# Kernel optimization log

Hardware: AMD Instinct MI355X
Metric: run time of the kernel (lower is better)

Reference implementation:

```python
import jax, jax.numpy as jnp
import numpy as np

K = 5          # kernel_size
PAD = (K - 1) // 2  # fixed_padding with dilation=1, stride=1 -> 'same'


def setup_inputs() -> dict:
    key = jax.random.key(0)
    kx, kw = jax.random.split(key)
    x = jax.random.normal(kx, (4, 8, 512, 512), dtype=jnp.float32)
    # nn.Parameter initialized to zeros in the original; use small random values
    # so the op is non-trivial (math is identical for any weight values).
    weight = jax.random.normal(kw, (8, 8, K, K), dtype=jnp.float32) * 0.05
    return {"x": x, "weight": weight}


def reference(x, weight):
    """Morphological dilation2d with hard max (soft_max=False).

    out[n,o,h,w] = max_{c,dy,dx} ( x_pad[n,c,h+dy,w+dx] + weight[o,c,dy,dx] )
    Faithful to: pad zeros -> unfold -> weight + x -> max over dim C*k*k.
    Computed as a fused sliding-window max-plus reduction (no (N,C,k,k,H,W)
    unfold tensor is materialized; loop is over the fixed k*k kernel taps).
    """
    N, C, H, W = x.shape
    O = weight.shape[0]
    xp = jnp.pad(x, ((0, 0), (0, 0), (PAD, PAD), (PAD, PAD)))  # zero pad, as in F.pad
    out = jnp.full((N, O, H, W), -jnp.inf, dtype=x.dtype)
    for dy in range(K):
        for dx in range(K):
            patch = xp[:, :, dy:dy + H, dx:dx + W]           # (N,C,H,W)
            w_tap = weight[:, :, dy, dx]                      # (O,C)
            # (N,1,C,H,W) + (1,O,C,1,1) -> max over C -> (N,O,H,W)
            term = patch[:, None] + w_tap[None, :, :, None, None]
            out = jnp.maximum(out, jnp.max(term, axis=2))
    return out
```

## Files before the change

### kernel.cpp

```cpp
#include <hip/hip_runtime.h>
#include <math.h>
#include <stdint.h>

#define KK 5
#define PADK 2
#define C_IN 8
#define O_OUT 8
#define HH 512
#define WW 512
#define TH 8
#define TW 128
#define LROWS 12
#define LCOLS 136
#define WSTR 16
#define NW (O_OUT * C_IN * KK * KK)
#define XPAIRS (C_IN * LROWS * (LCOLS / 2))

static __device__ __forceinline__ float max3f(float a, float b, float c) {
    float d;
    asm("v_max3_f32 %0, %1, %2, %3" : "=v"(d) : "v"(a), "v"(b), "v"(c));
    return d;
}

__global__ __launch_bounds__(512, 2)
void dil_kernel(const float* __restrict__ x,
                const float* __restrict__ wf,
                float* __restrict__ out) {
    __shared__ __align__(16) float xlds[C_IN][LROWS][LCOLS];
    __shared__ __align__(16) float wlds[C_IN * 4 * KK * WSTR];

    const int tid = threadIdx.x;
    const int w0 = blockIdx.x * TW;
    const int h0 = blockIdx.y * TH;
    const int n  = blockIdx.z;

    const float* xn = x + (size_t)n * (C_IN * HH * WW);
    for (int idx = tid; idx < XPAIRS; idx += 512) {
        int c   = idx / (LROWS * (LCOLS / 2));
        int rem = idx - c * (LROWS * (LCOLS / 2));
        int r   = rem / (LCOLS / 2);
        int jp  = rem - r * (LCOLS / 2);
        int gh = h0 - PADK + r;
        int gw = w0 - PADK + 2 * jp;
        float v0 = 0.f, v1 = 0.f;
        if ((unsigned)gh < (unsigned)HH) {
            const float* row = xn + ((size_t)c * HH + gh) * WW;
            if ((unsigned)gw < (unsigned)WW) v0 = row[gw];
            if ((unsigned)(gw + 1) < (unsigned)WW) v1 = row[gw + 1];
        }
        float2* dst = (float2*)&xlds[c][r][2 * jp];
        *dst = make_float2(v0, v1);
    }
    for (int t = tid; t < NW; t += 512) {
        int dx = t % KK;  int q = t / KK;
        int o2 = q & 1;   q >>= 1;
        int dy = q % KK;  q /= KK;
        int og = q & 3;   int c = q >> 2;
        int o = og * 2 + o2;
        wlds[((c * 4 + og) * KK + dy) * WSTR + o2 * KK + dx] =
            wf[((o * C_IN + c) * KK + dy) * KK + dx];
    }
    __syncthreads();

    const int l   = tid & 63;
    const int wid = tid >> 6;
    const int og  = wid & 3;
    const int rq  = wid >> 2;
    const int rbase = rq * 4;

    float acc[2][4][2];
    #pragma unroll
    for (int a = 0; a < 2; ++a)
        #pragma unroll
        for (int j = 0; j < 4; ++j) {
            acc[a][j][0] = -INFINITY;
            acc[a][j][1] = -INFINITY;
        }

    for (int c = 0; c < C_IN; ++c) {
        float U[8][6];
        #pragma unroll
        for (int r = 0; r < 8; ++r) {
            const float* lr = &xlds[c][rbase + r][2 * l];
            float2 a = *(const float2*)(lr);
            float2 b = *(const float2*)(lr + 2);
            float2 d = *(const float2*)(lr + 4);
            U[r][0] = a.x; U[r][1] = a.y;
            U[r][2] = b.x; U[r][3] = b.y;
            U[r][4] = d.x; U[r][5] = d.y;
        }
        const float* wb = &wlds[(c * 4 + og) * KK * WSTR];
        #pragma unroll
        for (int dy = 0; dy < KK; ++dy) {
            const float* wch = wb + dy * WSTR;
            float4 wa = *(const float4*)(wch);
            float4 wv = *(const float4*)(wch + 4);
            float2 wc2 = *(const float2*)(wch + 8);
            float w[10] = {wa.x, wa.y, wa.z, wa.w,
                           wv.x, wv.y, wv.z, wv.w, wc2.x, wc2.y};
            #pragma unroll
            for (int o2 = 0; o2 < 2; ++o2) {
                #pragma unroll
                for (int j = 0; j < 4; ++j) {
                    const float* u = U[j + dy];
                    const float* wo = &w[o2 * 5];
                    {
                        float t0 = u[0] + wo[0], t1 = u[1] + wo[1],
                              t2 = u[2] + wo[2], t3 = u[3] + wo[3],
                              t4 = u[4] + wo[4];
                        acc[o2][j][0] = max3f(acc[o2][j][0],
                                              max3f(t0, t1, t2),
                                              fmaxf(t3, t4));
                    }
                    {
                        float t0 = u[1] + wo[0], t1 = u[2] + wo[1],
                              t2 = u[3] + wo[2], t3 = u[4] + wo[3],
                              t4 = u[5] + wo[4];
                        acc[o2][j][1] = max3f(acc[o2][j][1],
                                              max3f(t0, t1, t2),
                                              fmaxf(t3, t4));
                    }
                }
            }
        }
    }

    float* onp = out + (size_t)n * (O_OUT * HH * WW);
    const int hB = h0 + rbase;
    const int wcol = w0 + 2 * l;
    #pragma unroll
    for (int o2 = 0; o2 < 2; ++o2) {
        const int o = og * 2 + o2;
        #pragma unroll
        for (int j = 0; j < 4; ++j) {
            float2 rr = make_float2(acc[o2][j][0], acc[o2][j][1]);
            *(float2*)(&onp[((size_t)o * HH + hB + j) * WW + wcol]) = rr;
        }
    }
}

extern "C" void kernel_launch(void* const* d_in, const int* in_sizes, int n_in,
                              void* d_out, int out_size, void* d_ws, size_t ws_size,
                              hipStream_t stream) {
    const float* x   = (const float*)d_in[0];
    const float* wgt = (const float*)d_in[1];
    float* out = (float*)d_out;

    dim3 grid(WW / TW, HH / TH, 4);
    dim3 block(512);
    dil_kernel<<<grid, block, 0, stream>>>(x, wgt, out);
}
```

Before: 69.13 us.

## Stage input channels in two halves to shrink LDS and raise occupancy

Loads the input tile into shared memory four channels at a time in two passes, which halves the LDS footprint, and tightens the weight stride from 16 to 12. The x rows are now read from LDS for each (dy, j) instead of being cached in a per-channel register array, and launch bounds ask for 8 blocks per CU. The aim is to raise occupancy and hide global-load latency through more resident waves. The cost is an extra barrier, a second load phase, more LDS reads (20 rows per channel instead of 8), and a tighter register budget that could cause spills.

```diff
diff --git a/kernel.cpp b/kernel.cpp
--- a/kernel.cpp
+++ b/kernel.cpp
@@ -10,11 +10,12 @@
 #define WW 512
 #define TH 8
 #define TW 128
+#define CH 4
 #define LROWS 12
 #define LCOLS 136
-#define WSTR 16
+#define WSTR 12
 #define NW (O_OUT * C_IN * KK * KK)
-#define XPAIRS (C_IN * LROWS * (LCOLS / 2))
+#define XHALF (CH * LROWS * (LCOLS / 2))
 
 static __device__ __forceinline__ float max3f(float a, float b, float c) {
     float d;
@@ -22,45 +23,18 @@
     return d;
 }
 
-__global__ __launch_bounds__(512, 2)
+__global__ __launch_bounds__(512, 8)
 void dil_kernel(const float* __restrict__ x,
                 const float* __restrict__ wf,
                 float* __restrict__ out) {
-    __shared__ __align__(16) float xlds[C_IN][LROWS][LCOLS];
+    __shared__ __align__(16) float xlds[CH][LROWS][LCOLS];
     __shared__ __align__(16) float wlds[C_IN * 4 * KK * WSTR];
 
     const int tid = threadIdx.x;
     const int w0 = blockIdx.x * TW;
     const int h0 = blockIdx.y * TH;
     const int n  = blockIdx.z;
-
     const float* xn = x + (size_t)n * (C_IN * HH * WW);
-    for (int idx = tid; idx < XPAIRS; idx += 512) {
-        int c   = idx / (LROWS * (LCOLS / 2));
-        int rem = idx - c * (LROWS * (LCOLS / 2));
-        int r   = rem / (LCOLS / 2);
-        int jp  = rem - r * (LCOLS / 2);
-        int gh = h0 - PADK + r;
-        int gw = w0 - PADK + 2 * jp;
-        float v0 = 0.f, v1 = 0.f;
-        if ((unsigned)gh < (unsigned)HH) {
-            const float* row = xn + ((size_t)c * HH + gh) * WW;
-            if ((unsigned)gw < (unsigned)WW) v0 = row[gw];
-            if ((unsigned)(gw + 1) < (unsigned)WW) v1 = row[gw + 1];
-        }
-        float2* dst = (float2*)&xlds[c][r][2 * jp];
-        *dst = make_float2(v0, v1);
-    }
-    for (int t = tid; t < NW; t += 512) {
-        int dx = t % KK;  int q = t / KK;
-        int o2 = q & 1;   q >>= 1;
-        int dy = q % KK;  q /= KK;
-        int og = q & 3;   int c = q >> 2;
-        int o = og * 2 + o2;
-        wlds[((c * 4 + og) * KK + dy) * WSTR + o2 * KK + dx] =
-            wf[((o * C_IN + c) * KK + dy) * KK + dx];
-    }
-    __syncthreads();
 
     const int l   = tid & 63;
     const int wid = tid >> 6;
@@ -77,48 +51,70 @@
             acc[a][j][1] = -INFINITY;
         }
 
-    for (int c = 0; c < C_IN; ++c) {
-        float U[8][6];
-        #pragma unroll
-        for (int r = 0; r < 8; ++r) {
-            const float* lr = &xlds[c][rbase + r][2 * l];
-            float2 a = *(const float2*)(lr);
-            float2 b = *(const float2*)(lr + 2);
-            float2 d = *(const float2*)(lr + 4);
-            U[r][0] = a.x; U[r][1] = a.y;
-            U[r][2] = b.x; U[r][3] = b.y;
-            U[r][4] = d.x; U[r][5] = d.y;
+    for (int h = 0; h < 2; ++h) {
+        if (h) __syncthreads();
+
+        for (int idx = tid; idx < XHALF; idx += 512) {
+            int cc  = idx / (LROWS * (LCOLS / 2));
+            int rem = idx - cc * (LROWS * (LCOLS / 2));
+            int r   = rem / (LCOLS / 2);
+            int jp  = rem - r * (LCOLS / 2);
+            int gh = h0 - PADK + r;
+            int gw = w0 - PADK + 2 * jp;
+            float v0 = 0.f, v1 = 0.f;
+            if ((unsigned)gh < (unsigned)HH) {
+                const float* row = xn + ((size_t)(h * CH + cc) * HH + gh) * WW;
+                if ((unsigned)gw < (unsigned)WW) v0 = row[gw];
+                if ((unsigned)(gw + 1) < (unsigned)WW) v1 = row[gw + 1];
+            }
+            *(float2*)&xlds[cc][r][2 * jp] = make_float2(v0, v1);
         }
-        const float* wb = &wlds[(c * 4 + og) * KK * WSTR];
-        #pragma unroll
-        for (int dy = 0; dy < KK; ++dy) {
-            const float* wch = wb + dy * WSTR;
-            float4 wa = *(const float4*)(wch);
-            float4 wv = *(const float4*)(wch + 4);
-            float2 wc2 = *(const float2*)(wch + 8);
-            float w[10] = {wa.x, wa.y, wa.z, wa.w,
-                           wv.x, wv.y, wv.z, wv.w, wc2.x, wc2.y};
+        if (h == 0) {
+            for (int t = tid; t < NW; t += 512) {
+                int dx = t % KK;  int q = t / KK;
+                int o2 = q & 1;   q >>= 1;
+                int dy = q % KK;  q /= KK;
+                int g  = q & 3;   int c = q >> 2;
+                int o = g * 2 + o2;
+                wlds[((c * 4 + g) * KK + dy) * WSTR + o2 * KK + dx] =
+                    wf[((o * C_IN + c) * KK + dy) * KK + dx];
+            }
+        }
+        __syncthreads();
+
+        for (int cc = 0; cc < CH; ++cc) {
+            const float* wb = &wlds[((h * CH + cc) * 4 + og) * KK * WSTR];
             #pragma unroll
-            for (int o2 = 0; o2 < 2; ++o2) {
+            for (int dy = 0; dy < KK; ++dy) {
+                const float* wch = wb + dy * WSTR;
+                float4 wa = *(const float4*)(wch);
+                float4 wv = *(const float4*)(wch + 4);
+                float2 wc2 = *(const float2*)(wch + 8);
+                const float w[10] = {wa.x, wa.y, wa.z, wa.w,
+                                     wv.x, wv.y, wv.z, wv.w, wc2.x, wc2.y};
                 #pragma unroll
                 for (int j = 0; j < 4; ++j) {
-                    const float* u = U[j + dy];
-                    const float* wo = &w[o2 * 5];
-                    {
-                        float t0 = u[0] + wo[0], t1 = u[1] + wo[1],
-                              t2 = u[2] + wo[2], t3 = u[3] + wo[3],
-                              t4 = u[4] + wo[4];
+                    const float* lr = &xlds[cc][rbase + dy + j][2 * l];
+                    float2 a = *(const float2*)(lr);
+                    float2 b = *(const float2*)(lr + 2);
+                    float2 d = *(const float2*)(lr + 4);
+                    const float u0 = a.x, u1 = a.y, u2 = b.x,
+                                u3 = b.y, u4 = d.x, u5 = d.y;
+                    #pragma unroll
+                    for (int o2 = 0; o2 < 2; ++o2) {
+                        const float* wo = &w[o2 * 5];
+                        float t0 = u0 + wo[0], t1 = u1 + wo[1],
+                              t2 = u2 + wo[2], t3 = u3 + wo[3],
+                              t4 = u4 + wo[4];
                         acc[o2][j][0] = max3f(acc[o2][j][0],
                                               max3f(t0, t1, t2),
                                               fmaxf(t3, t4));
-                    }
-                    {
-                        float t0 = u[1] + wo[0], t1 = u[2] + wo[1],
-                              t2 = u[3] + wo[2], t3 = u[4] + wo[3],
-                              t4 = u[5] + wo[4];
+                        float s0 = u1 + wo[0], s1 = u2 + wo[1],
+                              s2 = u3 + wo[2], s3 = u4 + wo[3],
+                              s4 = u5 + wo[4];
                         acc[o2][j][1] = max3f(acc[o2][j][1],
-                                              max3f(t0, t1, t2),
-                                              fmaxf(t3, t4));
+                                              max3f(s0, s1, s2),
+                                              fmaxf(s3, s4));
                     }
                 }
             }
```

After: 66.59 us. 3.7% less time.
